# Kernel optimization log

Hardware: AMD Instinct MI355X
Metric: run time of the kernel (lower is better)

Reference implementation:

```python
import jax, jax.numpy as jnp
import numpy as np

N, E, C, NE, G, T = 20000, 320000, 32, 10, 64, 1000
NB, HID, LAYERS = 8, 64, 2
R_MAX, P_CUT, AVG_NEIGH = 5.0, 6, 16.0
LM = 16  # (max_ell+1)^2 spherical-harmonic components
L_OF_LM = jnp.array([0,1,1,1,2,2,2,2,2,3,3,3,3,3,3,3])


def sph_harm(u):
    # component-normalized real spherical harmonics up to l=3 on unit vectors u [E,3]
    x, y, z = u[:, 0], u[:, 1], u[:, 2]
    s3, s15, s5, s105, s7 = 3**0.5, 15**0.5, 5**0.5, 105**0.5, 7**0.5
    s35_8, s21_8 = (35.0/8.0)**0.5, (21.0/8.0)**0.5
    comps = [jnp.ones_like(x),
             s3*x, s3*y, s3*z,
             s15*x*y, s15*y*z, 0.5*s5*(3*z*z-1.0), s15*x*z, 0.5*s15*(x*x-y*y),
             s35_8*y*(3*x*x-y*y), s105*x*y*z, s21_8*y*(5*z*z-1.0),
             0.5*s7*(5*z*z*z-3*z), s21_8*x*(5*z*z-1.0),
             0.5*s105*z*(x*x-y*y), s35_8*x*(x*x-3*y*y)]
    return jnp.stack(comps, axis=-1)  # [E,16]


def radial_embed(r):
    # Bessel basis with polynomial cutoff (MACE RadialEmbeddingBlock)
    n = jnp.arange(1, NB + 1, dtype=r.dtype)
    rc = jnp.maximum(r, 1e-9)
    bessel = (2.0/R_MAX)**0.5 * jnp.sin(n[None, :]*jnp.pi*rc[:, None]/R_MAX) / rc[:, None]
    xr = r / R_MAX
    p = float(P_CUT)
    f = (1.0 - 0.5*(p+1)*(p+2)*xr**p + p*(p+2)*xr**(p+1) - 0.5*p*(p+1)*xr**(p+2))
    f = f * (xr < 1.0)
    return bessel * f[:, None]  # [E,NB]


def setup_inputs():
    key = jax.random.key(0)
    ks = jax.random.split(key, 16)
    positions = jax.random.normal(ks[0], (N, 3)) * 3.0
    species = jax.random.randint(ks[1], (N,), 0, NE)
    node_attrs = jax.nn.one_hot(species, NE, dtype=jnp.float32)
    edge_index = jax.random.randint(ks[2], (2, E), 0, N)
    shifts = jnp.zeros((E, 3), jnp.float32)
    batch = jnp.sort(jax.random.randint(ks[3], (N,), 0, G))
    t = jax.random.randint(ks[4], (G,), 0, T)
    eps = jax.random.normal(ks[5], (N, NE + 3))
    betas = jnp.linspace(1e-4, 0.02, T)
    alpha_bar = jnp.cumprod(1.0 - betas)
    sc = 0.1
    W_embed = sc * jax.random.normal(ks[6], (NE + 1, C))
    W_r1 = sc * jax.random.normal(ks[7], (LAYERS, NB, HID))
    W_r2 = sc * jax.random.normal(ks[8], (LAYERS, HID, C * 4))
    W_mix = sc * jax.random.normal(ks[9], (LAYERS, 4, C, C))
    W_sc = sc * jax.random.normal(ks[10], (NE, C))
    W_prod = sc * jax.random.normal(ks[11], (LAYERS, 3, C))
    W_ro_s = sc * jax.random.normal(ks[12], (LAYERS, C, NE))
    W_ro_v = sc * jax.random.normal(ks[13], (LAYERS, C))
    return {"positions": positions, "node_attrs": node_attrs, "shifts": shifts,
            "eps": eps, "alpha_bar": alpha_bar, "W_embed": W_embed, "W_r1": W_r1,
            "W_r2": W_r2, "W_mix": W_mix, "W_sc": W_sc, "W_prod": W_prod,
            "W_ro_s": W_ro_s, "W_ro_v": W_ro_v, "edge_index": edge_index,
            "batch": batch, "t": t}


def reference(positions, node_attrs, shifts, eps, alpha_bar, W_embed, W_r1, W_r2,
              W_mix, W_sc, W_prod, W_ro_s, W_ro_v, edge_index, batch, t):
    sender, receiver = edge_index[0], edge_index[1]
    # diffusion: noise positions and attrs (DDPM q(x_t|x_0))
    ab = alpha_bar[t][batch][:, None]                       # [N,1]
    attrs0 = node_attrs / 4.0
    pos_noisy = jnp.sqrt(ab) * positions + jnp.sqrt(1.0 - ab) * eps[:, -3:]
    attrs_noisy = jnp.sqrt(ab) * attrs0 + jnp.sqrt(1.0 - ab) * eps[:, :NE]
    tf = (t.astype(jnp.float32) / T)[batch][:, None]
    h = jnp.concatenate([attrs_noisy, tf], axis=-1) @ W_embed  # [N,C]
    # edge geometry
    vec = pos_noisy[receiver] - pos_noisy[sender] + shifts
    r = jnp.sqrt(jnp.sum(vec * vec, axis=-1) + 1e-12)
    Y = sph_harm(vec / r[:, None])                          # [E,16]
    ef = radial_embed(r)                                    # [E,NB]
    scalar = h
    pred = jnp.zeros((N, NE + 3), h.dtype)
    for layer in range(LAYERS):
        rw = jax.nn.silu(ef @ W_r1[layer]) @ W_r2[layer]    # [E,4C]
        rw = rw.reshape(E, C, 4)[:, :, L_OF_LM]             # [E,C,16]
        msg = rw * scalar[sender][:, :, None] * Y[:, None, :]
        agg = jax.ops.segment_sum(msg, receiver, num_segments=N) / AVG_NEIGH
        Wm = W_mix[layer][L_OF_LM]                          # [16,C,C]
        feats = jnp.einsum('nck,kcd->ndk', agg, Wm)         # per-l channel mix
        s = feats[:, :, 0]
        poly = W_prod[layer, 0] + W_prod[layer, 1] * s + W_prod[layer, 2] * s * s
        feats = feats * poly[:, :, None]                    # correlation-3 product
        if layer == 0:
            feats = feats.at[:, :, 0].add(attrs_noisy @ W_sc)  # element skip
        scalar = feats[:, :, 0]
        pred_s = scalar @ W_ro_s[layer]                     # [N,NE]
        pred_v = jnp.einsum('ncm,c->nm', feats[:, :, 1:4], W_ro_v[layer])  # [N,3]
        pred = pred + jnp.concatenate([pred_s, pred_v], axis=-1)
    err = (pred - eps) ** 2
    loss_pos = jax.ops.segment_sum(err[:, -3:].sum(-1), batch, num_segments=G)
    loss_lab = jax.ops.segment_sum(err[:, :NE].sum(-1), batch, num_segments=G)
    nn = jax.ops.segment_sum(jnp.ones((N,), pred.dtype), batch, num_segments=G)
    loss = 0.5 * (loss_pos + loss_lab) / (jnp.maximum(nn, 1.0) * (3 + NE))
    return loss
```

## Files before the change

kernel.cpp:

```cpp
#include <hip/hip_runtime.h>

typedef unsigned short ushort_t;
typedef unsigned int uint_t;

#define NN 20000
#define EE 320000
#define CC 32
#define NEL 10
#define GG 64
#define TTT 1000
#define NBB 8
#define HIDD 64
#define EPB 256
#define NTILE (EE / 16)

typedef __attribute__((ext_vector_type(8))) short bf16x8;
typedef __attribute__((ext_vector_type(4))) float f32x4;

__device__ __forceinline__ float bits2f(uint_t b) { union { uint_t u; float f; } v; v.u = b; return v.f; }
__device__ __forceinline__ ushort_t f2b(float f) {
  union { float f; uint_t u; } v; v.f = f;
  uint_t r = (v.u + 0x7fffu + ((v.u >> 16) & 1u)) >> 16;
  return (ushort_t)r;
}
__device__ __forceinline__ uint_t pk(float a, float b) {
  return (uint_t)f2b(a) | ((uint_t)f2b(b) << 16);
}
__device__ __forceinline__ float lo16(uint_t u) { return bits2f(u << 16); }
__device__ __forceinline__ float hi16(uint_t u) { return bits2f(u & 0xffff0000u); }

__global__ __launch_bounds__(256) void k_prep(
    const float* __restrict__ positions, const float* __restrict__ node_attrs,
    const float* __restrict__ eps, const float* __restrict__ alpha_bar,
    const float* __restrict__ W_embed, const float* __restrict__ W_sc,
    const int* __restrict__ batch, const int* __restrict__ tarr,
    float* __restrict__ pos_noisy, float* __restrict__ scalA,
    float* __restrict__ sc_skip, float* __restrict__ pred, int* __restrict__ deg)
{
  int n = blockIdx.x * 256 + threadIdx.x;
  if (n >= NN) return;
  deg[n] = 0;
  int g = batch[n];
  int tn = tarr[g];
  float ab = alpha_bar[tn];
  float sa = sqrtf(ab), sb = sqrtf(fmaxf(1.0f - ab, 0.0f));
#pragma unroll
  for (int j = 0; j < 3; ++j)
    pos_noisy[n * 3 + j] = sa * positions[n * 3 + j] + sb * eps[n * 13 + 10 + j];
  float an[10];
#pragma unroll
  for (int j = 0; j < 10; ++j)
    an[j] = sa * 0.25f * node_attrs[n * 10 + j] + sb * eps[n * 13 + j];
  float tf = (float)tn * (1.0f / (float)TTT);
  for (int d = 0; d < CC; ++d) {
    float h = tf * W_embed[10 * CC + d];
    float sk = 0.0f;
#pragma unroll
    for (int j = 0; j < 10; ++j) {
      h = fmaf(an[j], W_embed[j * CC + d], h);
      sk = fmaf(an[j], W_sc[j * CC + d], sk);
    }
    scalA[n * CC + d] = h;
    sc_skip[n * CC + d] = sk;
  }
#pragma unroll
  for (int j = 0; j < 13; ++j) pred[n * 13 + j] = 0.0f;
}

__global__ __launch_bounds__(256) void k_wpack(const float* __restrict__ W_r2,
    const float* __restrict__ W_mix, ushort_t* __restrict__ w2tg,
    ushort_t* __restrict__ wmixb)
{
  int idx = blockIdx.x * 256 + threadIdx.x;
  if (idx < 16384) {
    int l = idx >> 13, r = idx & 8191;
    int n = r >> 6, k = r & 63;
    w2tg[idx] = f2b(W_r2[l * 8192 + k * 128 + n]);
  } else {
    int r = idx - 16384;
    int l = r >> 12, r2 = r & 4095;
    int col = r2 >> 5, ch = r2 & 31;
    int lq = col >> 5, d = col & 31;
    wmixb[r] = f2b(W_mix[l * 4096 + lq * 1024 + ch * 32 + d]);
  }
}

__global__ __launch_bounds__(256) void k_edge_deg(const int* __restrict__ ei,
    int* __restrict__ deg)
{
  int e = blockIdx.x * 256 + threadIdx.x;
  atomicAdd(&deg[ei[EE + e]], 1);
}

__global__ __launch_bounds__(1024) void k_scan(const int* __restrict__ deg,
    int* __restrict__ offs, int* __restrict__ cursor,
    float* __restrict__ lnum, float* __restrict__ lcnt)
{
  __shared__ int wsums[16];
  __shared__ int woffs[16];
  int tid = threadIdx.x, lane = tid & 63, wv = tid >> 6;
  if (tid < GG) { lnum[tid] = 0.0f; lcnt[tid] = 0.0f; }
  int base = tid * 20;
  int loc[20];
  int s = 0;
#pragma unroll
  for (int j = 0; j < 20; ++j) {
    int idx = base + j;
    int v = (idx < NN) ? deg[idx] : 0;
    loc[j] = s; s += v;
  }
  int inc = s;
  for (int o = 1; o < 64; o <<= 1) {
    int v = __shfl_up(inc, o, 64);
    if (lane >= o) inc += v;
  }
  if (lane == 63) wsums[wv] = inc;
  __syncthreads();
  if (wv == 0 && lane < 16) {
    int v = wsums[lane];
    int i2 = v;
    for (int o = 1; o < 16; o <<= 1) {
      int vv = __shfl_up(i2, o, 16);
      if (lane >= o) i2 += vv;
    }
    woffs[lane] = i2 - v;
  }
  __syncthreads();
  int texcl = woffs[wv] + (inc - s);
#pragma unroll
  for (int j = 0; j < 20; ++j) {
    int idx = base + j;
    if (idx < NN) { int v = texcl + loc[j]; offs[idx] = v; cursor[idx] = v; }
  }
  if (tid == 1023) offs[NN] = EE;
}

__global__ __launch_bounds__(256) void k_edge2(
    const float* __restrict__ pos_noisy, const float* __restrict__ shifts,
    const int* __restrict__ ei, int* __restrict__ cursor,
    ushort_t* __restrict__ Ys, ushort_t* __restrict__ efs, int* __restrict__ snds)
{
  int e = blockIdx.x * 256 + threadIdx.x;
  int snd = ei[e], rcv = ei[EE + e];
  float vx = pos_noisy[rcv * 3 + 0] - pos_noisy[snd * 3 + 0] + shifts[e * 3 + 0];
  float vy = pos_noisy[rcv * 3 + 1] - pos_noisy[snd * 3 + 1] + shifts[e * 3 + 1];
  float vz = pos_noisy[rcv * 3 + 2] - pos_noisy[snd * 3 + 2] + shifts[e * 3 + 2];
  float r2 = vx * vx + vy * vy + vz * vz + 1e-12f;
  float r = sqrtf(r2);
  float inv = 1.0f / r;
  float x = vx * inv, y = vy * inv, z = vz * inv;

  const float s3 = 1.7320508075688772f, s15 = 3.872983346207417f, s5 = 2.23606797749979f;
  const float s105 = 10.246950765959598f, s7 = 2.6457513110645907f;
  const float s35_8 = 2.091650066335189f, s21_8 = 1.6201851746019651f;
  float yv[16];
  yv[0] = 1.0f;
  yv[1] = s3 * x; yv[2] = s3 * y; yv[3] = s3 * z;
  yv[4] = s15 * x * y;
  yv[5] = s15 * y * z;
  yv[6] = 0.5f * s5 * (3.0f * z * z - 1.0f);
  yv[7] = s15 * x * z;
  yv[8] = 0.5f * s15 * (x * x - y * y);
  yv[9] = s35_8 * y * (3.0f * x * x - y * y);
  yv[10] = s105 * x * y * z;
  yv[11] = s21_8 * y * (5.0f * z * z - 1.0f);
  yv[12] = 0.5f * s7 * (5.0f * z * z * z - 3.0f * z);
  yv[13] = s21_8 * x * (5.0f * z * z - 1.0f);
  yv[14] = 0.5f * s105 * z * (x * x - y * y);
  yv[15] = s35_8 * x * (x * x - 3.0f * y * y);

  float rc = fmaxf(r, 1e-9f);
  float pref = 0.6324555320336759f / rc;
  float th = 0.6283185307179586f * rc;
  float s1 = __sinf(th), c1 = __cosf(th);
  float xr = r * 0.2f;
  float fcut = 0.0f;
  if (xr < 1.0f) {
    float x2 = xr * xr, x3 = x2 * xr;
    float x6 = x3 * x3, x7 = x6 * xr, x8 = x7 * xr;
    fcut = 1.0f - 28.0f * x6 + 48.0f * x7 - 21.0f * x8;
  }
  float efv[8];
  float sp = 0.0f, scur = s1, c2 = 2.0f * c1;
#pragma unroll
  for (int b = 0; b < 8; ++b) {
    efv[b] = pref * scur * fcut;
    float nx = c2 * scur - sp;
    sp = scur; scur = nx;
  }

  int slot = atomicAdd(&cursor[rcv], 1);
  snds[slot] = snd;
  uint4* Y4 = (uint4*)Ys;
  Y4[(size_t)slot * 2 + 0] = make_uint4(pk(yv[0], yv[1]), pk(yv[2], yv[3]),
                                        pk(yv[4], yv[5]), pk(yv[6], yv[7]));
  Y4[(size_t)slot * 2 + 1] = make_uint4(pk(yv[8], yv[9]), pk(yv[10], yv[11]),
                                        pk(yv[12], yv[13]), pk(yv[14], yv[15]));
  ((uint4*)efs)[slot] = make_uint4(pk(efv[0], efv[1]), pk(efv[2], efv[3]),
                                   pk(efv[4], efv[5]), pk(efv[6], efv[7]));
}

__global__ __launch_bounds__(256) void k_ytr(const ushort_t* __restrict__ Ys,
    ushort_t* __restrict__ YT)
{
  int idx = blockIdx.x * 256 + threadIdx.x;
  int tile = idx >> 4, k = idx & 15;
  ushort_t v[16];
#pragma unroll
  for (int el = 0; el < 16; ++el)
    v[el] = Ys[(size_t)(tile * 16 + el) * 16 + k];
  uint_t u[8];
#pragma unroll
  for (int p = 0; p < 8; ++p) u[p] = (uint_t)v[2 * p] | ((uint_t)v[2 * p + 1] << 16);
  uint4* o = (uint4*)(YT + (size_t)tile * 256 + (size_t)k * 16);
  o[0] = make_uint4(u[0], u[1], u[2], u[3]);
  o[1] = make_uint4(u[4], u[5], u[6], u[7]);
}

__global__ __launch_bounds__(256) void k_rw_mfma(
    const ushort_t* __restrict__ efs, const float* __restrict__ W_r1,
    const ushort_t* __restrict__ w2tg, const int* __restrict__ snds,
    const float* __restrict__ scal_in, ushort_t* __restrict__ rwT, int layer)
{
  __shared__ __align__(16) ushort_t h1[EPB][72];
  int tid = threadIdx.x;
  const float* W1g = W_r1 + layer * NBB * HIDD;
  const ushort_t* w2l = w2tg + layer * (HIDD * 128);
  {
    int e = blockIdx.x * EPB + tid;
    uint4 q = ((const uint4*)efs)[e];
    float efr[8] = {lo16(q.x), hi16(q.x), lo16(q.y), hi16(q.y),
                    lo16(q.z), hi16(q.z), lo16(q.w), hi16(q.w)};
    for (int hc = 0; hc < 8; ++hc) {
      float v[8];
#pragma unroll
      for (int hh = 0; hh < 8; ++hh) {
        int h = hc * 8 + hh;
        float t = 0.0f;
#pragma unroll
        for (int b = 0; b < 8; ++b) t = fmaf(efr[b], W1g[b * HIDD + h], t);
        v[hh] = t / (1.0f + __expf(-t));
      }
      *(uint4*)&h1[tid][hc * 8] = make_uint4(pk(v[0], v[1]), pk(v[2], v[3]),
                                             pk(v[4], v[5]), pk(v[6], v[7]));
    }
  }
  __builtin_amdgcn_wave_barrier();
  int w = tid >> 6, lane = tid & 63;
  int c = lane & 15, quad = lane >> 4;
  bf16x8 bfr[16];
#pragma unroll
  for (int nt = 0; nt < 8; ++nt)
#pragma unroll
    for (int kt = 0; kt < 2; ++kt)
      bfr[nt * 2 + kt] = *(const bf16x8*)&w2l[(nt * 16 + c) * 64 + kt * 32 + quad * 8];
  int mb0 = w * 64;
#pragma unroll
  for (int mt = 0; mt < 4; ++mt) {
    int mbase = mb0 + mt * 16;
    bf16x8 a0 = *(const bf16x8*)&h1[mbase + c][quad * 8];
    bf16x8 a1 = *(const bf16x8*)&h1[mbase + c][32 + quad * 8];
    size_t erow = (size_t)blockIdx.x * EPB + mbase + quad * 4;
    int4 sn = *(const int4*)&snds[erow];
    const float* sb0 = scal_in + (size_t)sn.x * CC;
    const float* sb1 = scal_in + (size_t)sn.y * CC;
    const float* sb2 = scal_in + (size_t)sn.z * CC;
    const float* sb3 = scal_in + (size_t)sn.w * CC;
    int tile = blockIdx.x * 16 + w * 4 + mt;
#pragma unroll
    for (int nt = 0; nt < 8; ++nt) {
      f32x4 acc = {0.0f, 0.0f, 0.0f, 0.0f};
      acc = __builtin_amdgcn_mfma_f32_16x16x32_bf16(a0, bfr[nt * 2 + 0], acc, 0, 0, 0);
      acc = __builtin_amdgcn_mfma_f32_16x16x32_bf16(a1, bfr[nt * 2 + 1], acc, 0, 0, 0);
      int col = nt * 16 + c;
      int cc = col >> 2;
      uint2 st;
      st.x = pk(acc[0] * sb0[cc], acc[1] * sb1[cc]);
      st.y = pk(acc[2] * sb2[cc], acc[3] * sb3[cc]);
      *(uint2*)(rwT + (size_t)tile * 2048 + (size_t)col * 16 + quad * 4) = st;
    }
  }
}

__global__ __launch_bounds__(256) void k_layer(
    const ushort_t* __restrict__ YT, const ushort_t* __restrict__ rwT,
    float* __restrict__ scal_out,
    const int* __restrict__ offs,
    const ushort_t* __restrict__ wmixb, const float* __restrict__ W_prod,
    const float* __restrict__ W_ro_s, const float* __restrict__ W_ro_v,
    const float* __restrict__ sc_skip, float* __restrict__ pred, int layer)
{
  __shared__ float lagg[4][CC][17];
  __shared__ float lfeat[4][CC][17];
  __shared__ float lf[4][CC][4];
  int w = threadIdx.x >> 6, lane = threadIdx.x & 63;
  int n = blockIdx.x * 4 + w;
  int c = lane & 15, quad = lane >> 4;
  int i0 = offs[n], i1 = offs[n + 1];
  int t0 = i0 >> 4, t1 = (i1 + 15) >> 4;
  int tsel = quad >> 1, half8 = quad & 1;
  f32x4 acc[8];
#pragma unroll
  for (int mt = 0; mt < 8; ++mt) acc[mt] = (f32x4){0.0f, 0.0f, 0.0f, 0.0f};

  for (int t = t0; t < t1; t += 2) {
    int ta = t + tsel;
    bf16x8 a[8];
    bf16x8 b;
    bool tv = (ta * 16 < i1) && (ta * 16 + 16 > i0);
    if (tv) {
      const bf16x8* ap = (const bf16x8*)rwT + (size_t)ta * 256 + c * 2 + half8;
#pragma unroll
      for (int mt = 0; mt < 8; ++mt) a[mt] = ap[mt * 32];
      b = ((const bf16x8*)YT)[(size_t)ta * 32 + c * 2 + half8];
      if (ta * 16 < i0 || ta * 16 + 16 > i1) {
        int sbase = ta * 16 + half8 * 8;
#pragma unroll
        for (int j = 0; j < 8; ++j) {
          int s = sbase + j;
          if (s < i0 || s >= i1) b[j] = 0;
        }
      }
    } else {
#pragma unroll
      for (int mt = 0; mt < 8; ++mt) a[mt] = (bf16x8){0, 0, 0, 0, 0, 0, 0, 0};
      b = (bf16x8){0, 0, 0, 0, 0, 0, 0, 0};
    }
#pragma unroll
    for (int mt = 0; mt < 8; ++mt)
      acc[mt] = __builtin_amdgcn_mfma_f32_16x16x32_bf16(a[mt], b, acc[mt], 0, 0, 0);
  }

  int lc = (c >= 1) + (c >= 4) + (c >= 9);
  const float inva = 1.0f / 16.0f;
#pragma unroll
  for (int mt = 0; mt < 8; ++mt) {
    float v = (lc == 0) ? acc[mt][0] : (lc == 1) ? acc[mt][1]
            : (lc == 2) ? acc[mt][2] : acc[mt][3];
    lagg[w][mt * 4 + quad][c] = v * inva;
  }
  __builtin_amdgcn_wave_barrier();

  float av[8];
#pragma unroll
  for (int j = 0; j < 8; ++j) av[j] = lagg[w][quad * 8 + j][c];
  union { uint_t u[4]; bf16x8 b; } cv;
  cv.u[0] = pk(av[0], av[1]); cv.u[1] = pk(av[2], av[3]);
  cv.u[2] = pk(av[4], av[5]); cv.u[3] = pk(av[6], av[7]);
  bf16x8 afrag = cv.b;
  const ushort_t* wmixl = wmixb + layer * 4096;
  f32x4 o[8];
#pragma unroll
  for (int nt = 0; nt < 8; ++nt) {
    bf16x8 bfm = *(const bf16x8*)&wmixl[(nt * 16 + c) * 32 + quad * 8];
    f32x4 z = {0.0f, 0.0f, 0.0f, 0.0f};
    o[nt] = __builtin_amdgcn_mfma_f32_16x16x32_bf16(afrag, bfm, z, 0, 0, 0);
  }
#pragma unroll
  for (int jj = 0; jj < 4; ++jj) {
    int k = quad * 4 + jj;
    int lq = (k >= 1) + (k >= 4) + (k >= 9);
    float vlo = (lq == 0) ? o[0][jj] : (lq == 1) ? o[2][jj]
              : (lq == 2) ? o[4][jj] : o[6][jj];
    float vhi = (lq == 0) ? o[1][jj] : (lq == 1) ? o[3][jj]
              : (lq == 2) ? o[5][jj] : o[7][jj];
    lfeat[w][c][k] = vlo;
    lfeat[w][c + 16][k] = vhi;
  }
  __builtin_amdgcn_wave_barrier();

  int d = lane >> 1;
  int kh = lane & 1;
  int kb = kh * 8;
  float ft[8];
#pragma unroll
  for (int j = 0; j < 8; ++j) ft[j] = lfeat[w][d][kb + j];
  float sv = lfeat[w][d][0];
  const float* Wp = W_prod + layer * 96;
  float p0 = Wp[d], p1 = Wp[32 + d], p2 = Wp[64 + d];
  float poly = fmaf(fmaf(p2, sv, p1), sv, p0);
#pragma unroll
  for (int j = 0; j < 8; ++j) ft[j] *= poly;
  if (layer == 0 && kh == 0) ft[0] += sc_skip[n * CC + d];
  if (kh == 0) {
    scal_out[n * CC + d] = ft[0];
    lf[w][d][0] = ft[0]; lf[w][d][1] = ft[1]; lf[w][d][2] = ft[2]; lf[w][d][3] = ft[3];
  }
  __builtin_amdgcn_wave_barrier();
  if (lane < 13) {
    float sum = 0.0f;
    if (lane < 10) {
      const float* Wr = W_ro_s + layer * CC * NEL;
      for (int dd = 0; dd < CC; ++dd) sum = fmaf(lf[w][dd][0], Wr[dd * NEL + lane], sum);
    } else {
      int mm = lane - 10;
      const float* Wv = W_ro_v + layer * CC;
      for (int dd = 0; dd < CC; ++dd) sum = fmaf(lf[w][dd][1 + mm], Wv[dd], sum);
    }
    pred[n * 13 + lane] += sum;
  }
}

__global__ __launch_bounds__(256) void k_loss(const float* __restrict__ pred,
    const float* __restrict__ eps, const int* __restrict__ batch,
    float* __restrict__ lnum, float* __restrict__ lcnt)
{
  __shared__ float psum[GG];
  __shared__ int pcnt[GG];
  int tid = threadIdx.x;
  if (tid < GG) { psum[tid] = 0.0f; pcnt[tid] = 0; }
  __syncthreads();
  int n = blockIdx.x * 256 + tid;
  if (n < NN) {
    int g = batch[n];
    float sum = 0.0f;
#pragma unroll
    for (int j = 0; j < 13; ++j) {
      float dlt = pred[n * 13 + j] - eps[n * 13 + j];
      sum = fmaf(dlt, dlt, sum);
    }
    atomicAdd(&psum[g], sum);
    atomicAdd(&pcnt[g], 1);
  }
  __syncthreads();
  if (tid < GG && pcnt[tid] > 0) {
    atomicAdd(&lnum[tid], psum[tid]);
    atomicAdd(&lcnt[tid], (float)pcnt[tid]);
  }
}

__global__ void k_final(const float* __restrict__ lnum, const float* __restrict__ lcnt,
    float* __restrict__ out)
{
  int g = threadIdx.x;
  if (g < GG) {
    float nn = fmaxf(lcnt[g], 1.0f);
    out[g] = 0.5f * lnum[g] / (nn * 13.0f);
  }
}

extern "C" void kernel_launch(void* const* d_in, const int* in_sizes, int n_in,
                              void* d_out, int out_size, void* d_ws, size_t ws_size,
                              hipStream_t stream) {
  const float* positions  = (const float*)d_in[0];
  const float* node_attrs = (const float*)d_in[1];
  const float* shifts     = (const float*)d_in[2];
  const float* eps        = (const float*)d_in[3];
  const float* alpha_bar  = (const float*)d_in[4];
  const float* W_embed    = (const float*)d_in[5];
  const float* W_r1       = (const float*)d_in[6];
  const float* W_r2       = (const float*)d_in[7];
  const float* W_mix      = (const float*)d_in[8];
  const float* W_sc       = (const float*)d_in[9];
  const float* W_prod     = (const float*)d_in[10];
  const float* W_ro_s     = (const float*)d_in[11];
  const float* W_ro_v     = (const float*)d_in[12];
  const int* edge_index   = (const int*)d_in[13];
  const int* batch        = (const int*)d_in[14];
  const int* tarr         = (const int*)d_in[15];
  float* out = (float*)d_out;

  char* ws = (char*)d_ws;
  size_t off = 0;
  auto alloc = [&](size_t bytes) -> void* {
    void* p = ws + off;
    off = (off + bytes + 255) & ~(size_t)255;
    return p;
  };
  float* pos_noisy = (float*)alloc(NN * 3 * 4);
  float* scalA     = (float*)alloc(NN * CC * 4);
  float* scalB     = (float*)alloc(NN * CC * 4);
  float* sc_skip   = (float*)alloc(NN * CC * 4);
  float* pred      = (float*)alloc(NN * 13 * 4);
  ushort_t* Ys     = (ushort_t*)alloc((size_t)EE * 16 * 2);
  ushort_t* YT     = (ushort_t*)alloc((size_t)EE * 16 * 2);
  ushort_t* efs    = (ushort_t*)alloc((size_t)EE * 8 * 2);
  int* snds        = (int*)alloc((size_t)EE * 4);
  ushort_t* rwT    = (ushort_t*)alloc((size_t)EE * 128 * 2);
  ushort_t* w2tg   = (ushort_t*)alloc(2 * HIDD * 128 * 2);
  ushort_t* wmixb  = (ushort_t*)alloc(2 * 128 * CC * 2);
  int* deg         = (int*)alloc(NN * 4);
  int* offs        = (int*)alloc((NN + 1) * 4);
  int* cursor      = (int*)alloc(NN * 4);
  float* lnum      = (float*)alloc(GG * 4);
  float* lcnt      = (float*)alloc(GG * 4);
  (void)ws_size; (void)in_sizes; (void)n_in; (void)out_size;

  const int NB_N = (NN + 255) / 256;
  const int NB_E = EE / 256;

  k_prep<<<NB_N, 256, 0, stream>>>(positions, node_attrs, eps, alpha_bar, W_embed,
                                   W_sc, batch, tarr, pos_noisy, scalA, sc_skip, pred, deg);
  k_wpack<<<96, 256, 0, stream>>>(W_r2, W_mix, w2tg, wmixb);
  k_edge_deg<<<NB_E, 256, 0, stream>>>(edge_index, deg);
  k_scan<<<1, 1024, 0, stream>>>(deg, offs, cursor, lnum, lcnt);
  k_edge2<<<NB_E, 256, 0, stream>>>(pos_noisy, shifts, edge_index, cursor, Ys, efs, snds);
  k_ytr<<<NB_E, 256, 0, stream>>>(Ys, YT);

  for (int layer = 0; layer < 2; ++layer) {
    const float* sin_p = (layer == 0) ? scalA : scalB;
    float* sout_p      = (layer == 0) ? scalB : scalA;
    k_rw_mfma<<<NB_E, 256, 0, stream>>>(efs, W_r1, w2tg, snds, sin_p, rwT, layer);
    k_layer<<<NN / 4, 256, 0, stream>>>(YT, rwT, sout_p, offs,
                                        wmixb, W_prod, W_ro_s, W_ro_v,
                                        sc_skip, pred, layer);
  }

  k_loss<<<NB_N, 256, 0, stream>>>(pred, eps, batch, lnum, lcnt);
  k_final<<<1, 64, 0, stream>>>(lnum, lcnt, out);
}
```

Baseline: 315.4 us.

## Use persistent grid-stride blocks, fold weight packing into prep, parallelize readout

Converts edge, transpose, radial-MLP and layer kernels to fixed-size grid-stride loops, so per-block setup such as the W_r2 fragment loads in k_rw_mfma is paid once per block and reused across many tiles. The weight-pack kernel is merged into k_prep as extra blocks, removing one launch. The per-node readout now spreads the 32-channel dot products across all 64 lanes and combines them with shuffles instead of leaving 13 lanes doing serial loops. Fewer, longer-lived blocks may hide latency less well and can leave the tail of the work unevenly balanced.

```diff
diff --git a/kernel.cpp b/kernel.cpp
--- a/kernel.cpp
+++ b/kernel.cpp
@@ -13,6 +13,9 @@
 #define HIDD 64
 #define EPB 256
 #define NTILE (EE / 16)
+#define GRID_RW 625
+#define GRID_E  625
+#define GRID_L  1250
 
 typedef __attribute__((ext_vector_type(8))) short bf16x8;
 typedef __attribute__((ext_vector_type(4))) float f32x4;
@@ -33,10 +36,27 @@
     const float* __restrict__ positions, const float* __restrict__ node_attrs,
     const float* __restrict__ eps, const float* __restrict__ alpha_bar,
     const float* __restrict__ W_embed, const float* __restrict__ W_sc,
+    const float* __restrict__ W_r2, const float* __restrict__ W_mix,
     const int* __restrict__ batch, const int* __restrict__ tarr,
     float* __restrict__ pos_noisy, float* __restrict__ scalA,
-    float* __restrict__ sc_skip, float* __restrict__ pred, int* __restrict__ deg)
-{
+    float* __restrict__ sc_skip, float* __restrict__ pred, int* __restrict__ deg,
+    ushort_t* __restrict__ w2tg, ushort_t* __restrict__ wmixb)
+{
+  if (blockIdx.x >= 79) {
+    int idx = (blockIdx.x - 79) * 256 + threadIdx.x;
+    if (idx < 16384) {
+      int l = idx >> 13, r = idx & 8191;
+      int n = r >> 6, k = r & 63;
+      w2tg[idx] = f2b(W_r2[l * 8192 + k * 128 + n]);
+    } else {
+      int r = idx - 16384;
+      int l = r >> 12, r2 = r & 4095;
+      int col = r2 >> 5, ch = r2 & 31;
+      int lq = col >> 5, d = col & 31;
+      wmixb[r] = f2b(W_mix[l * 4096 + lq * 1024 + ch * 32 + d]);
+    }
+    return;
+  }
   int n = blockIdx.x * 256 + threadIdx.x;
   if (n >= NN) return;
   deg[n] = 0;
@@ -67,29 +87,11 @@
   for (int j = 0; j < 13; ++j) pred[n * 13 + j] = 0.0f;
 }
 
-__global__ __launch_bounds__(256) void k_wpack(const float* __restrict__ W_r2,
-    const float* __restrict__ W_mix, ushort_t* __restrict__ w2tg,
-    ushort_t* __restrict__ wmixb)
-{
-  int idx = blockIdx.x * 256 + threadIdx.x;
-  if (idx < 16384) {
-    int l = idx >> 13, r = idx & 8191;
-    int n = r >> 6, k = r & 63;
-    w2tg[idx] = f2b(W_r2[l * 8192 + k * 128 + n]);
-  } else {
-    int r = idx - 16384;
-    int l = r >> 12, r2 = r & 4095;
-    int col = r2 >> 5, ch = r2 & 31;
-    int lq = col >> 5, d = col & 31;
-    wmixb[r] = f2b(W_mix[l * 4096 + lq * 1024 + ch * 32 + d]);
-  }
-}
-
 __global__ __launch_bounds__(256) void k_edge_deg(const int* __restrict__ ei,
     int* __restrict__ deg)
 {
-  int e = blockIdx.x * 256 + threadIdx.x;
-  atomicAdd(&deg[ei[EE + e]], 1);
+  for (int e = blockIdx.x * 256 + threadIdx.x; e < EE; e += 250 * 256)
+    atomicAdd(&deg[ei[EE + e]], 1);
 }
 
 __global__ __launch_bounds__(1024) void k_scan(const int* __restrict__ deg,
@@ -140,7 +142,7 @@
     const int* __restrict__ ei, int* __restrict__ cursor,
     ushort_t* __restrict__ Ys, ushort_t* __restrict__ efs, int* __restrict__ snds)
 {
-  int e = blockIdx.x * 256 + threadIdx.x;
+  for (int e = blockIdx.x * 256 + threadIdx.x; e < EE; e += GRID_E * 256) {
   int snd = ei[e], rcv = ei[EE + e];
   float vx = pos_noisy[rcv * 3 + 0] - pos_noisy[snd * 3 + 0] + shifts[e * 3 + 0];
   float vy = pos_noisy[rcv * 3 + 1] - pos_noisy[snd * 3 + 1] + shifts[e * 3 + 1];
@@ -198,12 +200,13 @@
                                         pk(yv[12], yv[13]), pk(yv[14], yv[15]));
   ((uint4*)efs)[slot] = make_uint4(pk(efv[0], efv[1]), pk(efv[2], efv[3]),
                                    pk(efv[4], efv[5]), pk(efv[6], efv[7]));
+  }
 }
 
 __global__ __launch_bounds__(256) void k_ytr(const ushort_t* __restrict__ Ys,
     ushort_t* __restrict__ YT)
 {
-  int idx = blockIdx.x * 256 + threadIdx.x;
+  for (int idx = blockIdx.x * 256 + threadIdx.x; idx < NTILE * 16; idx += GRID_E * 256) {
   int tile = idx >> 4, k = idx & 15;
   ushort_t v[16];
 #pragma unroll
@@ -215,6 +218,7 @@
   uint4* o = (uint4*)(YT + (size_t)tile * 256 + (size_t)k * 16);
   o[0] = make_uint4(u[0], u[1], u[2], u[3]);
   o[1] = make_uint4(u[4], u[5], u[6], u[7]);
+  }
 }
 
 __global__ __launch_bounds__(256) void k_rw_mfma(
@@ -226,8 +230,18 @@
   int tid = threadIdx.x;
   const float* W1g = W_r1 + layer * NBB * HIDD;
   const ushort_t* w2l = w2tg + layer * (HIDD * 128);
+  int w = tid >> 6, lane = tid & 63;
+  int c = lane & 15, quad = lane >> 4;
+  bf16x8 bfr[16];
+#pragma unroll
+  for (int nt = 0; nt < 8; ++nt)
+#pragma unroll
+    for (int kt = 0; kt < 2; ++kt)
+      bfr[nt * 2 + kt] = *(const bf16x8*)&w2l[(nt * 16 + c) * 64 + kt * 32 + quad * 8];
+
+  for (int eb = blockIdx.x; eb < EE / EPB; eb += GRID_RW) {
   {
-    int e = blockIdx.x * EPB + tid;
+    int e = eb * EPB + tid;
     uint4 q = ((const uint4*)efs)[e];
     float efr[8] = {lo16(q.x), hi16(q.x), lo16(q.y), hi16(q.y),
                     lo16(q.z), hi16(q.z), lo16(q.w), hi16(q.w)};
@@ -246,27 +260,19 @@
     }
   }
   __builtin_amdgcn_wave_barrier();
-  int w = tid >> 6, lane = tid & 63;
-  int c = lane & 15, quad = lane >> 4;
-  bf16x8 bfr[16];
-#pragma unroll
-  for (int nt = 0; nt < 8; ++nt)
-#pragma unroll
-    for (int kt = 0; kt < 2; ++kt)
-      bfr[nt * 2 + kt] = *(const bf16x8*)&w2l[(nt * 16 + c) * 64 + kt * 32 + quad * 8];
   int mb0 = w * 64;
 #pragma unroll
   for (int mt = 0; mt < 4; ++mt) {
     int mbase = mb0 + mt * 16;
     bf16x8 a0 = *(const bf16x8*)&h1[mbase + c][quad * 8];
     bf16x8 a1 = *(const bf16x8*)&h1[mbase + c][32 + quad * 8];
-    size_t erow = (size_t)blockIdx.x * EPB + mbase + quad * 4;
+    size_t erow = (size_t)eb * EPB + mbase + quad * 4;
     int4 sn = *(const int4*)&snds[erow];
     const float* sb0 = scal_in + (size_t)sn.x * CC;
     const float* sb1 = scal_in + (size_t)sn.y * CC;
     const float* sb2 = scal_in + (size_t)sn.z * CC;
     const float* sb3 = scal_in + (size_t)sn.w * CC;
-    int tile = blockIdx.x * 16 + w * 4 + mt;
+    int tile = eb * 16 + w * 4 + mt;
 #pragma unroll
     for (int nt = 0; nt < 8; ++nt) {
       f32x4 acc = {0.0f, 0.0f, 0.0f, 0.0f};
@@ -280,6 +286,8 @@
       *(uint2*)(rwT + (size_t)tile * 2048 + (size_t)col * 16 + quad * 4) = st;
     }
   }
+  __builtin_amdgcn_wave_barrier();
+  }
 }
 
 __global__ __launch_bounds__(256) void k_layer(
@@ -294,11 +302,13 @@
   __shared__ float lfeat[4][CC][17];
   __shared__ float lf[4][CC][4];
   int w = threadIdx.x >> 6, lane = threadIdx.x & 63;
-  int n = blockIdx.x * 4 + w;
   int c = lane & 15, quad = lane >> 4;
+  int tsel = quad >> 1, half8 = quad & 1;
+
+  for (int grp = blockIdx.x; grp < NN / 4; grp += GRID_L) {
+  int n = grp * 4 + w;
   int i0 = offs[n], i1 = offs[n + 1];
   int t0 = i0 >> 4, t1 = (i1 + 15) >> 4;
-  int tsel = quad >> 1, half8 = quad & 1;
   f32x4 acc[8];
 #pragma unroll
   for (int mt = 0; mt < 8; ++mt) acc[mt] = (f32x4){0.0f, 0.0f, 0.0f, 0.0f};
@@ -387,17 +397,32 @@
     lf[w][d][0] = ft[0]; lf[w][d][1] = ft[1]; lf[w][d][2] = ft[2]; lf[w][d][3] = ft[3];
   }
   __builtin_amdgcn_wave_barrier();
-  if (lane < 13) {
+  {
+    int p = lane >> 4, m = lane & 15;
     float sum = 0.0f;
-    if (lane < 10) {
-      const float* Wr = W_ro_s + layer * CC * NEL;
-      for (int dd = 0; dd < CC; ++dd) sum = fmaf(lf[w][dd][0], Wr[dd * NEL + lane], sum);
-    } else {
-      int mm = lane - 10;
-      const float* Wv = W_ro_v + layer * CC;
-      for (int dd = 0; dd < CC; ++dd) sum = fmaf(lf[w][dd][1 + mm], Wv[dd], sum);
-    }
-    pred[n * 13 + lane] += sum;
+    if (m < 13) {
+      if (m < 10) {
+        const float* Wr = W_ro_s + layer * CC * NEL;
+#pragma unroll
+        for (int q = 0; q < 8; ++q) {
+          int dd = p * 8 + q;
+          sum = fmaf(lf[w][dd][0], Wr[dd * NEL + m], sum);
+        }
+      } else {
+        int mm = m - 10;
+        const float* Wv = W_ro_v + layer * CC;
+#pragma unroll
+        for (int q = 0; q < 8; ++q) {
+          int dd = p * 8 + q;
+          sum = fmaf(lf[w][dd][1 + mm], Wv[dd], sum);
+        }
+      }
+    }
+    sum += __shfl_down(sum, 32, 64);
+    sum += __shfl_down(sum, 16, 64);
+    if (lane < 13) pred[n * 13 + lane] += sum;
+  }
+  __builtin_amdgcn_wave_barrier();
   }
 }
 
@@ -487,21 +512,21 @@
   (void)ws_size; (void)in_sizes; (void)n_in; (void)out_size;
 
   const int NB_N = (NN + 255) / 256;
-  const int NB_E = EE / 256;
-
-  k_prep<<<NB_N, 256, 0, stream>>>(positions, node_attrs, eps, alpha_bar, W_embed,
-                                   W_sc, batch, tarr, pos_noisy, scalA, sc_skip, pred, deg);
-  k_wpack<<<96, 256, 0, stream>>>(W_r2, W_mix, w2tg, wmixb);
-  k_edge_deg<<<NB_E, 256, 0, stream>>>(edge_index, deg);
+
+  k_prep<<<NB_N + 96, 256, 0, stream>>>(positions, node_attrs, eps, alpha_bar,
+                                        W_embed, W_sc, W_r2, W_mix, batch, tarr,
+                                        pos_noisy, scalA, sc_skip, pred, deg,
+                                        w2tg, wmixb);
+  k_edge_deg<<<250, 256, 0, stream>>>(edge_index, deg);
   k_scan<<<1, 1024, 0, stream>>>(deg, offs, cursor, lnum, lcnt);
-  k_edge2<<<NB_E, 256, 0, stream>>>(pos_noisy, shifts, edge_index, cursor, Ys, efs, snds);
-  k_ytr<<<NB_E, 256, 0, stream>>>(Ys, YT);
+  k_edge2<<<GRID_E, 256, 0, stream>>>(pos_noisy, shifts, edge_index, cursor, Ys, efs, snds);
+  k_ytr<<<GRID_E, 256, 0, stream>>>(Ys, YT);
 
   for (int layer = 0; layer < 2; ++layer) {
     const float* sin_p = (layer == 0) ? scalA : scalB;
     float* sout_p      = (layer == 0) ? scalB : scalA;
-    k_rw_mfma<<<NB_E, 256, 0, stream>>>(efs, W_r1, w2tg, snds, sin_p, rwT, layer);
-    k_layer<<<NN / 4, 256, 0, stream>>>(YT, rwT, sout_p, offs,
+    k_rw_mfma<<<GRID_RW, 256, 0, stream>>>(efs, W_r1, w2tg, snds, sin_p, rwT, layer);
+    k_layer<<<GRID_L, 256, 0, stream>>>(YT, rwT, sout_p, offs,
                                         wmixb, W_prod, W_ro_s, W_ro_v,
                                         sc_skip, pred, layer);
   }
```

Measured after the change: 379.9 us. 20.5% more time.
